# Kernel optimization log

Hardware: AMD Instinct MI355X
Metric: run time of the kernel (lower is better)

The kernel has to match this reference:

```python
import jax, jax.numpy as jnp
import numpy as np

TOP_K = 5
EPS = 1e-12

def _l2norm(x, axis=-1):
    n = jnp.sqrt(jnp.sum(x * x, axis=axis, keepdims=True))
    return x / jnp.maximum(n, EPS)

def setup_inputs() -> dict:
    key = jax.random.key(0)
    ks = jax.random.split(key, 6)
    B, S, D, N = 16, 2048, 512, 200000
    return {
        "hidden_states": jax.random.normal(ks[0], (B, S, D), dtype=jnp.float32),
        "doc_embeddings": jax.random.normal(ks[1], (N, D), dtype=jnp.float32),
        "W_q": jax.random.normal(ks[2], (D, D), dtype=jnp.float32) * 0.02,
        "b_q": jnp.zeros((D,), dtype=jnp.float32),
        "W_gate": jax.random.normal(ks[3], (D, 2 * D), dtype=jnp.float32) * 0.02,
        "b_gate": jnp.zeros((D,), dtype=jnp.float32),
    }

def reference(hidden_states, doc_embeddings, W_q, b_q, W_gate, b_gate):
    B, S, D = hidden_states.shape
    # set_doc_embeddings: cosine metric normalizes doc table once
    docs = _l2norm(doc_embeddings, axis=1)          # [N, D]
    # forward: mean-pool query, linear encode
    query = hidden_states.mean(axis=1)              # [B, D]
    query = query @ W_q.T + b_q                     # torch Linear: x @ W^T + b
    # cosine similarity scan over full corpus
    q = _l2norm(query, axis=1)                      # [B, D]
    scores_full = q @ docs.T                        # [B, N]  (memory-bound scan)
    top_scores, indices = jax.lax.top_k(scores_full, TOP_K)  # [B, K], [B, K]
    # fuse context (gate method)
    retrieved = docs[indices]                       # [B, K, D] gather
    weights = jax.nn.softmax(top_scores, axis=1)    # [B, K]
    context = jnp.einsum('bk,bkd->bd', weights, retrieved)   # [B, D]
    context_exp = jnp.broadcast_to(context[:, None, :], (B, S, D))
    combined = jnp.concatenate([hidden_states, context_exp], axis=-1)  # [B, S, 2D]
    gate = jax.nn.sigmoid(combined @ W_gate.T + b_gate)       # [B, S, D]
    fused = gate * hidden_states + (1.0 - gate) * context_exp
    return top_scores, indices, fused
```

## Files before the change

### kernel.cpp

```cpp
#include <hip/hip_runtime.h>
#include <hip/hip_bf16.h>
#include <math.h>

#define BB 16
#define SS 2048
#define DD 512
#define NDOCS 200000
#define TOPK 5
#define EPSN 1e-12f
#define NEG_INF (-3.0e38f)

#define NW 4096
#define NTILE 12500

typedef short s16x8 __attribute__((ext_vector_type(8)));
typedef float f32x4 __attribute__((ext_vector_type(4)));

__device__ __forceinline__ short f2bf(float f) {
    __bf16 b = (__bf16)f;
    short s;
    __builtin_memcpy(&s, &b, 2);
    return s;
}

__device__ __forceinline__ void gload_lds16(const void* g, void* l) {
    __builtin_amdgcn_global_load_lds(
        (const __attribute__((address_space(1))) void*)g,
        (__attribute__((address_space(3))) void*)l, 16, 0, 0);
}

__global__ __launch_bounds__(128) void k1_mean_partial(
    const float* __restrict__ hs, float* __restrict__ partial) {
    int b = blockIdx.y, sc = blockIdx.x;
    int t = threadIdx.x;
    const float4* src = (const float4*)(hs + (size_t)(b * SS + sc * 64) * DD);
    float4 acc = {0.f, 0.f, 0.f, 0.f};
    for (int s = 0; s < 64; ++s) {
        float4 v = src[(size_t)s * 128 + t];
        acc.x += v.x; acc.y += v.y; acc.z += v.z; acc.w += v.w;
    }
    ((float4*)partial)[(size_t)(sc * BB + b) * 128 + t] = acc;
}

__global__ __launch_bounds__(128) void k1b_mean_reduce(
    const float* __restrict__ partial, float* __restrict__ mean) {
    int b = blockIdx.y, jc = blockIdx.x;
    int j = jc * 128 + threadIdx.x;
    float s = 0.f;
    for (int c = 0; c < 32; ++c) s += partial[(size_t)(c * BB + b) * DD + j];
    mean[(size_t)b * DD + j] = s * (1.0f / 2048.0f);
}

__global__ __launch_bounds__(256) void k2a_q_gemv(
    const float* __restrict__ mean, const float* __restrict__ Wq,
    const float* __restrict__ bq, float* __restrict__ qtmp) {
    int b = blockIdx.y, jc = blockIdx.x;
    int t = threadIdx.x;
    int r = t >> 4, c = t & 15;
    int row = jc * 16 + r;
    const float4* wr = (const float4*)(Wq + (size_t)row * DD);
    const float4* mv = (const float4*)(mean + (size_t)b * DD);
    float acc = 0.f;
#pragma unroll
    for (int it = 0; it < 8; ++it) {
        int k4 = c + it * 16;
        float4 w = wr[k4], m = mv[k4];
        acc = fmaf(w.x, m.x, acc); acc = fmaf(w.y, m.y, acc);
        acc = fmaf(w.z, m.z, acc); acc = fmaf(w.w, m.w, acc);
    }
#pragma unroll
    for (int m = 1; m < 16; m <<= 1) acc += __shfl_xor(acc, m);
    if (c == 0) qtmp[(size_t)b * DD + row] = acc + bq[row];
}

__global__ __launch_bounds__(256) void k2b_q_norm(
    const float* __restrict__ qtmp, float* __restrict__ qv) {
    int b = blockIdx.x, t = threadIdx.x;
    __shared__ float red[4];
    float a0 = qtmp[(size_t)b * DD + t];
    float a1 = qtmp[(size_t)b * DD + t + 256];
    float ss = a0 * a0 + a1 * a1;
#pragma unroll
    for (int m = 1; m < 64; m <<= 1) ss += __shfl_xor(ss, m);
    if ((t & 63) == 0) red[t >> 6] = ss;
    __syncthreads();
    float inv = 1.0f / fmaxf(sqrtf(red[0] + red[1] + red[2] + red[3]), EPSN);
    qv[(size_t)b * DD + t] = a0 * inv;
    qv[(size_t)b * DD + t + 256] = a1 * inv;
}

__global__ __launch_bounds__(256) void k2c_qsplit(
    const float* __restrict__ qv, short* __restrict__ qsplit) {
    int b = blockIdx.x, t = threadIdx.x;
#pragma unroll
    for (int kk = 0; kk < 2; ++kk) {
        int k = t + kk * 256;
        float f = qv[(size_t)b * DD + k];
        unsigned u = __float_as_uint(f);
        short hi = (short)(u >> 16);
        float r = f - __uint_as_float(u & 0xFFFF0000u);
        short lo = f2bf(r);
        int slot = k >> 3, j = k & 7;
        int off = b * 512 + ((slot ^ (b & 7)) << 3) + j;
        qsplit[off] = hi;
        qsplit[8192 + off] = lo;
    }
}

__global__ __launch_bounds__(256, 4) void k3_scores(
    const float* __restrict__ docs, const short* __restrict__ qsplit,
    float* __restrict__ cand_s, int* __restrict__ cand_i) {
    __shared__ short qS[2 * 8192];

    int t = threadIdx.x;
    int w = t >> 6, lane = t & 63;
    int bq = lane & 15, kg = lane >> 4;

#pragma unroll
    for (int j = 0; j < 8; ++j) {
        int u = ((w * 8 + j) << 6) + lane;
        gload_lds16(qsplit + (size_t)u * 8, (void*)&qS[(w * 8 + j) * 512]);
    }
    __syncthreads();

    int gw = blockIdx.x * 4 + w;

    float lv[TOPK]; int li[TOPK];
#pragma unroll
    for (int r = 0; r < TOPK; ++r) { lv[r] = NEG_INF; li[r] = 0x7fffffff; }

    auto ins = [&](float s, int di) {
        if (s > lv[4] || (s == lv[4] && di < li[4])) {
            lv[4] = s; li[4] = di;
#pragma unroll
            for (int k = 4; k > 0; --k) {
                if (lv[k] > lv[k - 1] || (lv[k] == lv[k - 1] && li[k] < li[k - 1])) {
                    float tv = lv[k]; lv[k] = lv[k - 1]; lv[k - 1] = tv;
                    int   ti = li[k]; li[k] = li[k - 1]; li[k - 1] = ti;
                }
            }
        }
    };

    for (int tt = gw; tt < NTILE; tt += NW) {
        const float4* dp = (const float4*)docs + (size_t)(tt * 16 + bq) * 128 + kg * 2;
        f32x4 acc = {0.f, 0.f, 0.f, 0.f};
        f32x4 n1  = {0.f, 0.f, 0.f, 0.f};
        f32x4 n2  = {0.f, 0.f, 0.f, 0.f};

        auto proc = [&](int c, float4 e0, float4 e1) {
            int qoff = ((((c * 4 + kg) ^ (bq & 7)) << 3)) + bq * 512;
            s16x8 qh = *(const s16x8*)&qS[qoff];
            s16x8 ql = *(const s16x8*)&qS[8192 + qoff];
            float ef[8] = {e0.x, e0.y, e0.z, e0.w, e1.x, e1.y, e1.z, e1.w};
            s16x8 ah, al;
#pragma unroll
            for (int i = 0; i < 8; ++i) {
                unsigned u = __float_as_uint(ef[i]);
                ah[i] = (short)(u >> 16);
                al[i] = f2bf(ef[i] - __uint_as_float(u & 0xFFFF0000u));
            }
            acc = __builtin_amdgcn_mfma_f32_16x16x32_bf16(ah, qh, acc, 0, 0, 0);
            acc = __builtin_amdgcn_mfma_f32_16x16x32_bf16(ah, ql, acc, 0, 0, 0);
            acc = __builtin_amdgcn_mfma_f32_16x16x32_bf16(al, qh, acc, 0, 0, 0);
            n1  = __builtin_amdgcn_mfma_f32_16x16x32_bf16(ah, ah, n1, 0, 0, 0);
            n2  = __builtin_amdgcn_mfma_f32_16x16x32_bf16(ah, al, n2, 0, 0, 0);
        };

        float4 a0 = dp[0], a1 = dp[1];
        float4 b0 = dp[8], b1 = dp[9];
#pragma unroll
        for (int c = 0; c < 16; c += 2) {
            proc(c, a0, a1);
            if (c + 2 < 16) { a0 = dp[(c + 2) * 8]; a1 = dp[(c + 2) * 8 + 1]; }
            proc(c + 1, b0, b1);
            if (c + 3 < 16) { b0 = dp[(c + 3) * 8]; b1 = dp[(c + 3) * 8 + 1]; }
        }

        int rd = bq & 3;
        float nd = n1[rd] + 2.0f * n2[rd];
        float invn = 1.0f / fmaxf(sqrtf(nd), EPSN);
#pragma unroll
        for (int r = 0; r < 4; ++r) {
            float iv = __shfl(invn, kg * 20 + r);
            float s = acc[r] * iv;
            int di = tt * 16 + kg * 4 + r;
            ins(s, di);
        }
    }

#pragma unroll
    for (int step = 16; step <= 32; step <<= 1) {
        float ov[TOPK]; int oi[TOPK];
#pragma unroll
        for (int r = 0; r < TOPK; ++r) {
            ov[r] = __shfl_xor(lv[r], step);
            oi[r] = __shfl_xor(li[r], step);
        }
#pragma unroll
        for (int r = 0; r < TOPK; ++r) ins(ov[r], oi[r]);
    }

    if (kg == 0) {
#pragma unroll
        for (int r = 0; r < TOPK; ++r) {
            cand_s[((long)gw * BB + bq) * TOPK + r] = lv[r];
            cand_i[((long)gw * BB + bq) * TOPK + r] = li[r];
        }
    }
}

__global__ __launch_bounds__(256) void k4a_topk_ctx(
    const float* __restrict__ docs, const float* __restrict__ cand_s,
    const int* __restrict__ cand_i, float* __restrict__ ctx,
    float* __restrict__ outp) {
    int b = blockIdx.x, t = threadIdx.x;
    __shared__ float sv[256];
    __shared__ int   si[256];
    __shared__ float topv[TOPK];
    __shared__ int   topi[TOPK];
    __shared__ float red[4];
    __shared__ float nrm5[TOPK];
    __shared__ float wts[TOPK];

    float lv[TOPK]; int li[TOPK];
#pragma unroll
    for (int r = 0; r < TOPK; ++r) { lv[r] = NEG_INF; li[r] = 0x7fffffff; }

    for (int j = t; j < NW * TOPK; j += 256) {
        int blk = j / TOPK, r = j - blk * TOPK;
        float s = cand_s[(long)blk * (BB * TOPK) + b * TOPK + r];
        int  di = cand_i[(long)blk * (BB * TOPK) + b * TOPK + r];
        if (s > lv[TOPK - 1] || (s == lv[TOPK - 1] && di < li[TOPK - 1])) {
            lv[TOPK - 1] = s; li[TOPK - 1] = di;
#pragma unroll
            for (int k = TOPK - 1; k > 0; --k) {
                if (lv[k] > lv[k - 1] || (lv[k] == lv[k - 1] && li[k] < li[k - 1])) {
                    float tv = lv[k]; lv[k] = lv[k - 1]; lv[k - 1] = tv;
                    int   ti = li[k]; li[k] = li[k - 1]; li[k - 1] = ti;
                }
            }
        }
    }

    int p = 0;
    for (int r = 0; r < TOPK; ++r) {
        float hv = (p < TOPK) ? lv[p] : NEG_INF;
        int   hi = (p < TOPK) ? li[p] : 0x7fffffff;
        sv[t] = hv; si[t] = hi;
        __syncthreads();
        for (int off = 128; off > 0; off >>= 1) {
            if (t < off) {
                float ov = sv[t + off]; int oi = si[t + off];
                if (ov > sv[t] || (ov == sv[t] && oi < si[t])) { sv[t] = ov; si[t] = oi; }
            }
            __syncthreads();
        }
        if (t == 0) { topv[r] = sv[0]; topi[r] = si[0]; }
        __syncthreads();
        if (hv == topv[r] && hi == topi[r]) ++p;
        __syncthreads();
    }

    for (int r = 0; r < TOPK; ++r) {
        const float* dr = docs + (size_t)topi[r] * DD;
        float s2 = dr[t] * dr[t] + dr[t + 256] * dr[t + 256];
#pragma unroll
        for (int m = 1; m < 64; m <<= 1) s2 += __shfl_xor(s2, m);
        if ((t & 63) == 0) red[t >> 6] = s2;
        __syncthreads();
        if (t == 0) nrm5[r] = sqrtf(red[0] + red[1] + red[2] + red[3]);
        __syncthreads();
    }

    if (t == 0) {
        float m = topv[0];
        float e[TOPK], s = 0.f;
#pragma unroll
        for (int r = 0; r < TOPK; ++r) { e[r] = expf(topv[r] - m); s += e[r]; }
#pragma unroll
        for (int r = 0; r < TOPK; ++r) wts[r] = e[r] / s;
    }
    __syncthreads();

    for (int j = t; j < DD; j += 256) {
        float c = 0.f;
#pragma unroll
        for (int r = 0; r < TOPK; ++r)
            c += wts[r] * docs[(size_t)topi[r] * DD + j] / fmaxf(nrm5[r], EPSN);
        ctx[(size_t)b * DD + j] = c;
    }

    if (t < TOPK) {
        outp[b * TOPK + t] = topv[t];
        outp[BB * TOPK + b * TOPK + t] = (float)topi[t];
    }
}

__global__ __launch_bounds__(256) void k4b_ctxb_gemv(
    const float* __restrict__ ctx, const float* __restrict__ Wg,
    const float* __restrict__ bgt, float* __restrict__ ctxb) {
    int b = blockIdx.y, jc = blockIdx.x;
    int t = threadIdx.x;
    int r = t >> 4, c = t & 15;
    int row = jc * 16 + r;
    const float4* wr = (const float4*)(Wg + (size_t)row * (2 * DD) + DD);
    const float4* mv = (const float4*)(ctx + (size_t)b * DD);
    float acc = 0.f;
#pragma unroll
    for (int it = 0; it < 8; ++it) {
        int k4 = c + it * 16;
        float4 w = wr[k4], m = mv[k4];
        acc = fmaf(w.x, m.x, acc); acc = fmaf(w.y, m.y, acc);
        acc = fmaf(w.z, m.z, acc); acc = fmaf(w.w, m.w, acc);
    }
#pragma unroll
    for (int m = 1; m < 16; m <<= 1) acc += __shfl_xor(acc, m);
    if (c == 0) ctxb[(size_t)b * DD + row] = acc + bgt[row];
}

#define BK 32
__global__ __launch_bounds__(512, 2) void k5_gemm_fused(
    const float* __restrict__ hs, const float* __restrict__ Wg,
    const float* __restrict__ ctx, const float* __restrict__ ctxb,
    float* __restrict__ outF) {
    __shared__ short At[128][BK];
    __shared__ short Bt[512][BK];
    __shared__ float ctxLds[DD];
    __shared__ float ctxbLds[DD];

    int bm = blockIdx.x;
    int t = threadIdx.x;
    int wv = t >> 6, lane = t & 63, ln = lane & 15, kg = lane >> 4;
    int wm = (wv >> 2) * 64, wn = (wv & 3) * 128;
    int bbatch = bm >> 4;

    ctxLds[t]  = ctx[(size_t)bbatch * DD + t];
    ctxbLds[t] = ctxb[(size_t)bbatch * DD + t];

    float4 pf[5][2];
    auto gload = [&](int kt) {
        {
            const float* src = hs + (size_t)(bm * 128 + (t >> 2)) * DD + kt * BK + (t & 3) * 8;
            pf[0][0] = ((const float4*)src)[0];
            pf[0][1] = ((const float4*)src)[1];
        }
#pragma unroll
        for (int i = 0; i < 4; ++i) {
            int u = t + i * 512;
            const float* src = Wg + (size_t)(u >> 2) * (2 * DD) + kt * BK + (u & 3) * 8;
            pf[1 + i][0] = ((const float4*)src)[0];
            pf[1 + i][1] = ((const float4*)src)[1];
        }
    };
    auto cvt1 = [&](float4 lo, float4 hi) {
        s16x8 cv;
        cv[0] = f2bf(lo.x); cv[1] = f2bf(lo.y); cv[2] = f2bf(lo.z); cv[3] = f2bf(lo.w);
        cv[4] = f2bf(hi.x); cv[5] = f2bf(hi.y); cv[6] = f2bf(hi.z); cv[7] = f2bf(hi.w);
        return cv;
    };
    auto cvtwrite = [&]() {
        {
            int row = t >> 2, slot = t & 3;
            int sl = slot ^ ((row >> 1) & 3);
            *(s16x8*)(&At[row][sl * 8]) = cvt1(pf[0][0], pf[0][1]);
        }
#pragma unroll
        for (int i = 0; i < 4; ++i) {
            int u = t + i * 512;
            int row = u >> 2, slot = u & 3;
            int sl = slot ^ ((row >> 1) & 3);
            *(s16x8*)(&Bt[row][sl * 8]) = cvt1(pf[1 + i][0], pf[1 + i][1]);
        }
    };

    f32x4 accv[4][8];
#pragma unroll
    for (int i = 0; i < 4; ++i)
#pragma unroll
        for (int j = 0; j < 8; ++j) accv[i][j] = (f32x4){0.f, 0.f, 0.f, 0.f};

    gload(0);
    for (int kt = 0; kt < DD / BK; ++kt) {
        __syncthreads();
        cvtwrite();
        if (kt + 1 < DD / BK) gload(kt + 1);
        __syncthreads();
        s16x8 af[4], bfr[8];
#pragma unroll
        for (int mi = 0; mi < 4; ++mi) {
            int row = wm + mi * 16 + ln;
            int sl = kg ^ ((row >> 1) & 3);
            af[mi] = *(const s16x8*)&At[row][sl * 8];
        }
#pragma unroll
        for (int nj = 0; nj < 8; ++nj) {
            int row = wn + nj * 16 + ln;
            int sl = kg ^ ((row >> 1) & 3);
            bfr[nj] = *(const s16x8*)&Bt[row][sl * 8];
        }
#pragma unroll
        for (int mi = 0; mi < 4; ++mi)
#pragma unroll
            for (int nj = 0; nj < 8; ++nj)
                accv[mi][nj] = __builtin_amdgcn_mfma_f32_16x16x32_bf16(
                    af[mi], bfr[nj], accv[mi][nj], 0, 0, 0);
    }

#pragma unroll
    for (int mi = 0; mi < 4; ++mi)
#pragma unroll
        for (int nj = 0; nj < 8; ++nj)
#pragma unroll
            for (int r = 0; r < 4; ++r) {
                int ri = wm + mi * 16 + kg * 4 + r;
                int ci = wn + nj * 16 + ln;
                size_t grow = (size_t)bm * 128 + ri;
                float logit = accv[mi][nj][r] + ctxbLds[ci];
                float g = __builtin_amdgcn_rcpf(1.0f + __expf(-logit));
                float h = hs[grow * DD + ci];
                float cx = ctxLds[ci];
                outF[grow * DD + ci] = g * h + (1.0f - g) * cx;
            }
}

extern "C" void kernel_launch(void* const* d_in, const int* in_sizes, int n_in,
                              void* d_out, int out_size, void* d_ws, size_t ws_size,
                              hipStream_t stream) {
    const float* hs   = (const float*)d_in[0];
    const float* docs = (const float*)d_in[1];
    const float* Wq   = (const float*)d_in[2];
    const float* bq   = (const float*)d_in[3];
    const float* Wg   = (const float*)d_in[4];
    const float* bgt  = (const float*)d_in[5];
    float* outp = (float*)d_out;
    float* ws = (float*)d_ws;

    float* partial = ws;
    float* mean    = partial + 32 * BB * DD;
    float* qtmp    = mean + BB * DD;
    float* qv      = qtmp + BB * DD;
    float* ctx     = qv + BB * DD;
    float* ctxb    = ctx + BB * DD;
    float* cand_s  = ctxb + BB * DD;
    int*   cand_i  = (int*)(cand_s + (size_t)NW * BB * TOPK);
    short* qsplit  = (short*)(cand_i + (size_t)NW * BB * TOPK);

    k1_mean_partial<<<dim3(32, BB), 128, 0, stream>>>(hs, partial);
    k1b_mean_reduce<<<dim3(4, BB), 128, 0, stream>>>(partial, mean);
    k2a_q_gemv<<<dim3(32, BB), 256, 0, stream>>>(mean, Wq, bq, qtmp);
    k2b_q_norm<<<BB, 256, 0, stream>>>(qtmp, qv);
    k2c_qsplit<<<BB, 256, 0, stream>>>(qv, qsplit);
    k3_scores<<<NW / 4, 256, 0, stream>>>(docs, qsplit, cand_s, cand_i);
    k4a_topk_ctx<<<BB, 256, 0, stream>>>(docs, cand_s, cand_i, ctx, outp);
    k4b_ctxb_gemv<<<dim3(32, BB), 256, 0, stream>>>(ctx, Wg, bgt, ctxb);
    k5_gemm_fused<<<256, 512, 0, stream>>>(hs, Wg, ctx, ctxb,
                                           outp + 2 * BB * TOPK);
}
```

Before: 288.9 us.

## Replace split-bf16 MFMA doc scoring with plain fp32 FMA register-tiled scan

Rewrites the corpus-scoring kernel so it no longer splits docs and queries into hi/lo bf16 parts for three MFMAs plus two norm MFMAs. It computes exact fp32 dot products with scalar FMAs over a 4-doc by 16-query register tile, using a swizzled fp32 query layout in LDS and a butterfly shuffle reduction across lanes. It also adds explicit double-buffered prefetch of the next doc chunk and cuts the grid from 1024 to 768 blocks with occupancy 3. The goal is to drop conversion overhead and keep the memory-bound scan streaming, at the cost of more VALU work and heavier shuffle traffic.

After: 694.7 us. +140.4%, slower.

```diff
diff --git a/kernel.cpp b/kernel.cpp
--- a/kernel.cpp
+++ b/kernel.cpp
@@ -10,8 +10,9 @@
 #define EPSN 1e-12f
 #define NEG_INF (-3.0e38f)
 
-#define NW 4096
-#define NTILE 12500
+#define NBLK3 768
+#define NW (NBLK3 * 4)
+#define NTILE (NDOCS / 16)
 
 typedef short s16x8 __attribute__((ext_vector_type(8)));
 typedef float f32x4 __attribute__((ext_vector_type(4)));
@@ -89,39 +90,42 @@
     qv[(size_t)b * DD + t + 256] = a1 * inv;
 }
 
-__global__ __launch_bounds__(256) void k2c_qsplit(
-    const float* __restrict__ qv, short* __restrict__ qsplit) {
-    int b = blockIdx.x, t = threadIdx.x;
-#pragma unroll
-    for (int kk = 0; kk < 2; ++kk) {
-        int k = t + kk * 256;
-        float f = qv[(size_t)b * DD + k];
-        unsigned u = __float_as_uint(f);
-        short hi = (short)(u >> 16);
-        float r = f - __uint_as_float(u & 0xFFFF0000u);
-        short lo = f2bf(r);
-        int slot = k >> 3, j = k & 7;
-        int off = b * 512 + ((slot ^ (b & 7)) << 3) + j;
-        qsplit[off] = hi;
-        qsplit[8192 + off] = lo;
-    }
-}
-
-__global__ __launch_bounds__(256, 4) void k3_scores(
-    const float* __restrict__ docs, const short* __restrict__ qsplit,
+__global__ __launch_bounds__(512) void k2c_qsplit(
+    const float* __restrict__ qv, float* __restrict__ qphys) {
+    int k = threadIdx.x;
+    int j = k >> 6, dgrp = (k >> 2) & 15, e = k & 3;
+    int edg = (dgrp >> 2) & 3, gdg = dgrp & 3;
+    int base = j * 1024 + dgrp * 64 + ((e ^ edg) << 4);
+#pragma unroll
+    for (int b = 0; b < BB; ++b) {
+        int g = b >> 2, bi = b & 3;
+        qphys[base + (((g ^ gdg)) << 2) + bi] = qv[(size_t)b * DD + k];
+    }
+}
+
+__global__ __launch_bounds__(256, 3) void k3_scores(
+    const float* __restrict__ docs, const float* __restrict__ qphys,
     float* __restrict__ cand_s, int* __restrict__ cand_i) {
-    __shared__ short qS[2 * 8192];
+    __shared__ float qS[8192];
 
     int t = threadIdx.x;
     int w = t >> 6, lane = t & 63;
-    int bq = lane & 15, kg = lane >> 4;
-
-#pragma unroll
-    for (int j = 0; j < 8; ++j) {
-        int u = ((w * 8 + j) << 6) + lane;
-        gload_lds16(qsplit + (size_t)u * 8, (void*)&qS[(w * 8 + j) * 512]);
+    int rgrp = lane >> 4, dgrp = lane & 15;
+
+#pragma unroll
+    for (int jj = 0; jj < 8; ++jj) {
+        int u = ((w * 8 + jj) << 6) + lane;
+        gload_lds16(qphys + (size_t)u * 4, (void*)&qS[(w * 8 + jj) * 256]);
     }
     __syncthreads();
+
+    int edg = (dgrp >> 2) & 3, gdg = dgrp & 3;
+    int qoffs[4][4];
+#pragma unroll
+    for (int e = 0; e < 4; ++e)
+#pragma unroll
+        for (int g = 0; g < 4; ++g)
+            qoffs[e][g] = dgrp * 64 + ((e ^ edg) << 4) + ((g ^ gdg) << 2);
 
     int gw = blockIdx.x * 4 + w;
 
@@ -142,50 +146,102 @@
         }
     };
 
-    for (int tt = gw; tt < NTILE; tt += NW) {
-        const float4* dp = (const float4*)docs + (size_t)(tt * 16 + bq) * 128 + kg * 2;
-        f32x4 acc = {0.f, 0.f, 0.f, 0.f};
-        f32x4 n1  = {0.f, 0.f, 0.f, 0.f};
-        f32x4 n2  = {0.f, 0.f, 0.f, 0.f};
-
-        auto proc = [&](int c, float4 e0, float4 e1) {
-            int qoff = ((((c * 4 + kg) ^ (bq & 7)) << 3)) + bq * 512;
-            s16x8 qh = *(const s16x8*)&qS[qoff];
-            s16x8 ql = *(const s16x8*)&qS[8192 + qoff];
-            float ef[8] = {e0.x, e0.y, e0.z, e0.w, e1.x, e1.y, e1.z, e1.w};
-            s16x8 ah, al;
-#pragma unroll
-            for (int i = 0; i < 8; ++i) {
-                unsigned u = __float_as_uint(ef[i]);
-                ah[i] = (short)(u >> 16);
-                al[i] = f2bf(ef[i] - __uint_as_float(u & 0xFFFF0000u));
-            }
-            acc = __builtin_amdgcn_mfma_f32_16x16x32_bf16(ah, qh, acc, 0, 0, 0);
-            acc = __builtin_amdgcn_mfma_f32_16x16x32_bf16(ah, ql, acc, 0, 0, 0);
-            acc = __builtin_amdgcn_mfma_f32_16x16x32_bf16(al, qh, acc, 0, 0, 0);
-            n1  = __builtin_amdgcn_mfma_f32_16x16x32_bf16(ah, ah, n1, 0, 0, 0);
-            n2  = __builtin_amdgcn_mfma_f32_16x16x32_bf16(ah, al, n2, 0, 0, 0);
-        };
-
-        float4 a0 = dp[0], a1 = dp[1];
-        float4 b0 = dp[8], b1 = dp[9];
-#pragma unroll
-        for (int c = 0; c < 16; c += 2) {
-            proc(c, a0, a1);
-            if (c + 2 < 16) { a0 = dp[(c + 2) * 8]; a1 = dp[(c + 2) * 8 + 1]; }
-            proc(c + 1, b0, b1);
-            if (c + 3 < 16) { b0 = dp[(c + 3) * 8]; b1 = dp[(c + 3) * 8 + 1]; }
-        }
-
-        int rd = bq & 3;
-        float nd = n1[rd] + 2.0f * n2[rd];
-        float invn = 1.0f / fmaxf(sqrtf(nd), EPSN);
-#pragma unroll
-        for (int r = 0; r < 4; ++r) {
-            float iv = __shfl(invn, kg * 20 + r);
-            float s = acc[r] * iv;
-            int di = tt * 16 + kg * 4 + r;
-            ins(s, di);
+    auto loadrr = [&](long tt, int j, f32x4* dst) {
+        const float* p = docs + ((size_t)tt * 16 + rgrp) * DD + j * 64 + dgrp * 4;
+        dst[0] = *(const f32x4*)(p);
+        dst[1] = *(const f32x4*)(p + 2048);
+        dst[2] = *(const f32x4*)(p + 4096);
+        dst[3] = *(const f32x4*)(p + 6144);
+    };
+
+    int p0 = dgrp & 1, p1 = (dgrp >> 1) & 1, p2 = (dgrp >> 2) & 1, p3 = (dgrp >> 3) & 1;
+
+    f32x4 cur[4], nxt[4];
+    if (gw < NTILE) loadrr(gw, 0, cur);
+
+    for (long tt = gw; tt < NTILE; tt += NW) {
+        long ttn = (tt + NW < NTILE) ? tt + NW : tt;
+
+        f32x4 acc[4][4];
+        float nrm[4];
+#pragma unroll
+        for (int rr = 0; rr < 4; ++rr) {
+            nrm[rr] = 0.f;
+#pragma unroll
+            for (int g = 0; g < 4; ++g) acc[rr][g] = (f32x4){0.f, 0.f, 0.f, 0.f};
+        }
+
+#pragma unroll
+        for (int j = 0; j < 8; ++j) {
+            if (j < 7) loadrr(tt, j + 1, nxt);
+            else       loadrr(ttn, 0, nxt);
+            const float* qj = qS + j * 1024;
+#pragma unroll
+            for (int e = 0; e < 4; ++e) {
+#pragma unroll
+                for (int rr = 0; rr < 4; ++rr)
+                    nrm[rr] = fmaf(cur[rr][e], cur[rr][e], nrm[rr]);
+#pragma unroll
+                for (int g = 0; g < 4; ++g) {
+                    f32x4 qq = *(const f32x4*)(qj + qoffs[e][g]);
+#pragma unroll
+                    for (int rr = 0; rr < 4; ++rr) {
+                        float ee = cur[rr][e];
+                        acc[rr][g][0] = fmaf(ee, qq[0], acc[rr][g][0]);
+                        acc[rr][g][1] = fmaf(ee, qq[1], acc[rr][g][1]);
+                        acc[rr][g][2] = fmaf(ee, qq[2], acc[rr][g][2]);
+                        acc[rr][g][3] = fmaf(ee, qq[3], acc[rr][g][3]);
+                    }
+                }
+            }
+#pragma unroll
+            for (int rr = 0; rr < 4; ++rr) cur[rr] = nxt[rr];
+        }
+
+        float n1r[4][8];
+#pragma unroll
+        for (int rr = 0; rr < 4; ++rr)
+#pragma unroll
+            for (int bh = 0; bh < 8; ++bh) {
+                int g = bh >> 1, c0 = 2 * (bh & 1);
+                float tx   = p0 ? acc[rr][g][c0]     : acc[rr][g][c0 + 1];
+                float mine = p0 ? acc[rr][g][c0 + 1] : acc[rr][g][c0];
+                n1r[rr][bh] = mine + __shfl_xor(tx, 1);
+            }
+        float n2r[4][4];
+#pragma unroll
+        for (int rr = 0; rr < 4; ++rr)
+#pragma unroll
+            for (int bq = 0; bq < 4; ++bq) {
+                float tx   = p1 ? n1r[rr][2 * bq]     : n1r[rr][2 * bq + 1];
+                float mine = p1 ? n1r[rr][2 * bq + 1] : n1r[rr][2 * bq];
+                n2r[rr][bq] = mine + __shfl_xor(tx, 2);
+            }
+        float n3r[4][2];
+#pragma unroll
+        for (int rr = 0; rr < 4; ++rr)
+#pragma unroll
+            for (int bo = 0; bo < 2; ++bo) {
+                float tx   = p2 ? n2r[rr][2 * bo]     : n2r[rr][2 * bo + 1];
+                float mine = p2 ? n2r[rr][2 * bo + 1] : n2r[rr][2 * bo];
+                n3r[rr][bo] = mine + __shfl_xor(tx, 4);
+            }
+        float red[4];
+#pragma unroll
+        for (int rr = 0; rr < 4; ++rr) {
+            float tx   = p3 ? n3r[rr][0] : n3r[rr][1];
+            float mine = p3 ? n3r[rr][1] : n3r[rr][0];
+            red[rr] = mine + __shfl_xor(tx, 8);
+        }
+#pragma unroll
+        for (int m = 1; m < 16; m <<= 1)
+#pragma unroll
+            for (int rr = 0; rr < 4; ++rr) nrm[rr] += __shfl_xor(nrm[rr], m);
+
+#pragma unroll
+        for (int rr = 0; rr < 4; ++rr) {
+            float sc = red[rr] / fmaxf(sqrtf(nrm[rr]), EPSN);
+            ins(sc, (int)(tt * 16 + 4 * rr + rgrp));
         }
     }
 
@@ -201,11 +257,11 @@
         for (int r = 0; r < TOPK; ++r) ins(ov[r], oi[r]);
     }
 
-    if (kg == 0) {
+    if (rgrp == 0) {
 #pragma unroll
         for (int r = 0; r < TOPK; ++r) {
-            cand_s[((long)gw * BB + bq) * TOPK + r] = lv[r];
-            cand_i[((long)gw * BB + bq) * TOPK + r] = li[r];
+            cand_s[((long)gw * BB + dgrp) * TOPK + r] = lv[r];
+            cand_i[((long)gw * BB + dgrp) * TOPK + r] = li[r];
         }
     }
 }
@@ -444,14 +500,14 @@
     float* ctxb    = ctx + BB * DD;
     float* cand_s  = ctxb + BB * DD;
     int*   cand_i  = (int*)(cand_s + (size_t)NW * BB * TOPK);
-    short* qsplit  = (short*)(cand_i + (size_t)NW * BB * TOPK);
+    float* qphys   = (float*)(cand_i + (size_t)NW * BB * TOPK);
 
     k1_mean_partial<<<dim3(32, BB), 128, 0, stream>>>(hs, partial);
     k1b_mean_reduce<<<dim3(4, BB), 128, 0, stream>>>(partial, mean);
     k2a_q_gemv<<<dim3(32, BB), 256, 0, stream>>>(mean, Wq, bq, qtmp);
     k2b_q_norm<<<BB, 256, 0, stream>>>(qtmp, qv);
-    k2c_qsplit<<<BB, 256, 0, stream>>>(qv, qsplit);
-    k3_scores<<<NW / 4, 256, 0, stream>>>(docs, qsplit, cand_s, cand_i);
+    k2c_qsplit<<<1, 512, 0, stream>>>(qv, qphys);
+    k3_scores<<<NBLK3, 256, 0, stream>>>(docs, qphys, cand_s, cand_i);
     k4a_topk_ctx<<<BB, 256, 0, stream>>>(docs, cand_s, cand_i, ctx, outp);
     k4b_ctxb_gemv<<<dim3(32, BB), 256, 0, stream>>>(ctx, Wg, bgt, ctxb);
     k5_gemm_fused<<<256, 512, 0, stream>>>(hs, Wg, ctx, ctxb,
```

## Fold query split into score kernel, prefetch next tile, use VALU norms

Applied to the files above, without the earlier changes.

Removes the separate qsplit kernel: each score block now converts the normalized query into hi/lo bf16 parts in padded LDS itself. The doc scan uses fewer persistent waves (782 blocks) with a register pipeline that prefetches the first rows of the next tile across iterations. Doc norms are computed with scalar FMAs and cross-lane shuffles instead of two extra MFMAs, and the dot product is split into two accumulators. This trims a launch and MFMA work and aims to hide load latency, at the cost of redundant per-block query conversion and lower occupancy from dropping the launch-bounds hint.

Measured after the change: 257.3 us. 11.0% less time.

```diff
diff --git a/kernel.cpp b/kernel.cpp
--- a/kernel.cpp
+++ b/kernel.cpp
@@ -10,8 +10,10 @@
 #define EPSN 1e-12f
 #define NEG_INF (-3.0e38f)
 
-#define NW 4096
-#define NTILE 12500
+#define NB3 782
+#define NW3 (NB3 * 4)
+#define NT3 (NDOCS / 16)
+#define QSTR 520
 
 typedef short s16x8 __attribute__((ext_vector_type(8)));
 typedef float f32x4 __attribute__((ext_vector_type(4)));
@@ -89,37 +91,21 @@
     qv[(size_t)b * DD + t + 256] = a1 * inv;
 }
 
-__global__ __launch_bounds__(256) void k2c_qsplit(
-    const float* __restrict__ qv, short* __restrict__ qsplit) {
-    int b = blockIdx.x, t = threadIdx.x;
-#pragma unroll
-    for (int kk = 0; kk < 2; ++kk) {
-        int k = t + kk * 256;
-        float f = qv[(size_t)b * DD + k];
-        unsigned u = __float_as_uint(f);
-        short hi = (short)(u >> 16);
-        float r = f - __uint_as_float(u & 0xFFFF0000u);
-        short lo = f2bf(r);
-        int slot = k >> 3, j = k & 7;
-        int off = b * 512 + ((slot ^ (b & 7)) << 3) + j;
-        qsplit[off] = hi;
-        qsplit[8192 + off] = lo;
-    }
-}
-
-__global__ __launch_bounds__(256, 4) void k3_scores(
-    const float* __restrict__ docs, const short* __restrict__ qsplit,
+__global__ __launch_bounds__(256) void k3_scores(
+    const float* __restrict__ docs, const float* __restrict__ qv,
     float* __restrict__ cand_s, int* __restrict__ cand_i) {
-    __shared__ short qS[2 * 8192];
+    __shared__ short qS[2][BB * QSTR];
 
     int t = threadIdx.x;
     int w = t >> 6, lane = t & 63;
     int bq = lane & 15, kg = lane >> 4;
 
-#pragma unroll
-    for (int j = 0; j < 8; ++j) {
-        int u = ((w * 8 + j) << 6) + lane;
-        gload_lds16(qsplit + (size_t)u * 8, (void*)&qS[(w * 8 + j) * 512]);
+    for (int u = t; u < BB * DD; u += 256) {
+        int b = u >> 9, k = u & 511;
+        float f = qv[u];
+        unsigned uu = __float_as_uint(f);
+        qS[0][b * QSTR + k] = (short)(uu >> 16);
+        qS[1][b * QSTR + k] = f2bf(f - __uint_as_float(uu & 0xFFFF0000u));
     }
     __syncthreads();
 
@@ -142,51 +128,63 @@
         }
     };
 
-    for (int tt = gw; tt < NTILE; tt += NW) {
-        const float4* dp = (const float4*)docs + (size_t)(tt * 16 + bq) * 128 + kg * 2;
-        f32x4 acc = {0.f, 0.f, 0.f, 0.f};
-        f32x4 n1  = {0.f, 0.f, 0.f, 0.f};
-        f32x4 n2  = {0.f, 0.f, 0.f, 0.f};
-
-        auto proc = [&](int c, float4 e0, float4 e1) {
-            int qoff = ((((c * 4 + kg) ^ (bq & 7)) << 3)) + bq * 512;
-            s16x8 qh = *(const s16x8*)&qS[qoff];
-            s16x8 ql = *(const s16x8*)&qS[8192 + qoff];
-            float ef[8] = {e0.x, e0.y, e0.z, e0.w, e1.x, e1.y, e1.z, e1.w};
+    const short* qh_base = &qS[0][bq * QSTR + kg * 8];
+    const short* ql_base = &qS[1][bq * QSTR + kg * 8];
+
+    long tt = gw;
+    const float* dpt = docs + ((long)tt * 16 + bq) * DD + kg * 8;
+    f32x4 A0 = *(const f32x4*)(dpt);
+    f32x4 A1 = *(const f32x4*)(dpt + 4);
+    f32x4 B0 = *(const f32x4*)(dpt + 32);
+    f32x4 B1 = *(const f32x4*)(dpt + 36);
+
+    while (tt < NT3) {
+        long tt2 = (tt + NW3 < NT3) ? tt + NW3 : tt;
+        const float* dpn = docs + (tt2 * 16 + bq) * DD + kg * 8;
+
+        f32x4 acc1 = {0.f, 0.f, 0.f, 0.f};
+        f32x4 acc2 = {0.f, 0.f, 0.f, 0.f};
+        float nrm = 0.f;
+
+#pragma unroll
+        for (int c = 0; c < 16; ++c) {
+            f32x4 C0, C1;
+            if (c + 2 < 16) {
+                C0 = *(const f32x4*)(dpt + (c + 2) * 32);
+                C1 = *(const f32x4*)(dpt + (c + 2) * 32 + 4);
+            } else {
+                C0 = *(const f32x4*)(dpn + (c - 14) * 32);
+                C1 = *(const f32x4*)(dpn + (c - 14) * 32 + 4);
+            }
+            float ef[8] = {A0[0], A0[1], A0[2], A0[3], A1[0], A1[1], A1[2], A1[3]};
             s16x8 ah, al;
 #pragma unroll
             for (int i = 0; i < 8; ++i) {
                 unsigned u = __float_as_uint(ef[i]);
                 ah[i] = (short)(u >> 16);
                 al[i] = f2bf(ef[i] - __uint_as_float(u & 0xFFFF0000u));
-            }
-            acc = __builtin_amdgcn_mfma_f32_16x16x32_bf16(ah, qh, acc, 0, 0, 0);
-            acc = __builtin_amdgcn_mfma_f32_16x16x32_bf16(ah, ql, acc, 0, 0, 0);
-            acc = __builtin_amdgcn_mfma_f32_16x16x32_bf16(al, qh, acc, 0, 0, 0);
-            n1  = __builtin_amdgcn_mfma_f32_16x16x32_bf16(ah, ah, n1, 0, 0, 0);
-            n2  = __builtin_amdgcn_mfma_f32_16x16x32_bf16(ah, al, n2, 0, 0, 0);
-        };
-
-        float4 a0 = dp[0], a1 = dp[1];
-        float4 b0 = dp[8], b1 = dp[9];
-#pragma unroll
-        for (int c = 0; c < 16; c += 2) {
-            proc(c, a0, a1);
-            if (c + 2 < 16) { a0 = dp[(c + 2) * 8]; a1 = dp[(c + 2) * 8 + 1]; }
-            proc(c + 1, b0, b1);
-            if (c + 3 < 16) { b0 = dp[(c + 3) * 8]; b1 = dp[(c + 3) * 8 + 1]; }
-        }
-
-        int rd = bq & 3;
-        float nd = n1[rd] + 2.0f * n2[rd];
-        float invn = 1.0f / fmaxf(sqrtf(nd), EPSN);
+                nrm = fmaf(ef[i], ef[i], nrm);
+            }
+            s16x8 qh = *(const s16x8*)(qh_base + c * 32);
+            s16x8 ql = *(const s16x8*)(ql_base + c * 32);
+            acc1 = __builtin_amdgcn_mfma_f32_16x16x32_bf16(ah, qh, acc1, 0, 0, 0);
+            acc2 = __builtin_amdgcn_mfma_f32_16x16x32_bf16(ah, ql, acc2, 0, 0, 0);
+            acc2 = __builtin_amdgcn_mfma_f32_16x16x32_bf16(al, qh, acc2, 0, 0, 0);
+            A0 = B0; A1 = B1; B0 = C0; B1 = C1;
+        }
+
+        float nn = nrm + __shfl_xor(nrm, 16);
+        nn += __shfl_xor(nn, 32);
+        float invn = 1.0f / fmaxf(sqrtf(nn), EPSN);
+        f32x4 acct = acc1 + acc2;
 #pragma unroll
         for (int r = 0; r < 4; ++r) {
-            float iv = __shfl(invn, kg * 20 + r);
-            float s = acc[r] * iv;
-            int di = tt * 16 + kg * 4 + r;
-            ins(s, di);
-        }
+            float iv = __shfl(invn, kg * 4 + r);
+            ins(acct[r] * iv, (int)(tt * 16 + kg * 4 + r));
+        }
+
+        tt += NW3;
+        dpt = dpn;
     }
 
 #pragma unroll
@@ -227,7 +225,7 @@
 #pragma unroll
     for (int r = 0; r < TOPK; ++r) { lv[r] = NEG_INF; li[r] = 0x7fffffff; }
 
-    for (int j = t; j < NW * TOPK; j += 256) {
+    for (int j = t; j < NW3 * TOPK; j += 256) {
         int blk = j / TOPK, r = j - blk * TOPK;
         float s = cand_s[(long)blk * (BB * TOPK) + b * TOPK + r];
         int  di = cand_i[(long)blk * (BB * TOPK) + b * TOPK + r];
@@ -443,15 +441,13 @@
     float* ctx     = qv + BB * DD;
     float* ctxb    = ctx + BB * DD;
     float* cand_s  = ctxb + BB * DD;
-    int*   cand_i  = (int*)(cand_s + (size_t)NW * BB * TOPK);
-    short* qsplit  = (short*)(cand_i + (size_t)NW * BB * TOPK);
+    int*   cand_i  = (int*)(cand_s + (size_t)NW3 * BB * TOPK);
 
     k1_mean_partial<<<dim3(32, BB), 128, 0, stream>>>(hs, partial);
     k1b_mean_reduce<<<dim3(4, BB), 128, 0, stream>>>(partial, mean);
     k2a_q_gemv<<<dim3(32, BB), 256, 0, stream>>>(mean, Wq, bq, qtmp);
     k2b_q_norm<<<BB, 256, 0, stream>>>(qtmp, qv);
-    k2c_qsplit<<<BB, 256, 0, stream>>>(qv, qsplit);
-    k3_scores<<<NW / 4, 256, 0, stream>>>(docs, qsplit, cand_s, cand_i);
+    k3_scores<<<NB3, 256, 0, stream>>>(docs, qv, cand_s, cand_i);
     k4a_topk_ctx<<<BB, 256, 0, stream>>>(docs, cand_s, cand_i, ctx, outp);
     k4b_ctxb_gemv<<<dim3(32, BB), 256, 0, stream>>>(ctx, Wg, bgt, ctxb);
     k5_gemm_fused<<<256, 512, 0, stream>>>(hs, Wg, ctx, ctxb,
```
